# Performance work log

Hardware: AMD Instinct MI355X
Metric: run time of the kernel (lower is better)

## Reference

```python
import jax, jax.numpy as jnp
import numpy as np

B, L, SEQ_D, PAIR_D = 4, 512, 640, 128
C, H, NL = 128, 4, 3
DH = C // H
ED = PAIR_D + 1
KNN_K = 16
E_MAX = 131072
MIN_LOOP, MIN_PROB, HP_THRESH = 4, 0.01, 0.3


def _nussinov_pairs_np(P, min_loop=MIN_LOOP, min_prob=MIN_PROB):
    # Faithful numpy port of the torch.jit Nussinov DP (vectorized over diagonals)
    Ln = P.shape[0]
    S = np.zeros((Ln, Ln), dtype=np.float64)
    lo = np.where(P >= min_prob, np.log(P / (1.0 - P + 1e-9)), 0.0)
    for d in range(min_loop + 1, Ln):
        i = np.arange(Ln - d); j = i + d
        cand = np.maximum(np.maximum(S[i + 1, j], S[i, j - 1]), S[i + 1, j - 1] + lo[i, j])
        cand = np.maximum(cand, 0.0)  # best_bif starts at 0
        if d - min_loop - 1 > 0:
            K = np.arange(1, d - min_loop)
            bif = (S[i[:, None], i[:, None] + K[None, :]] + S[i[:, None] + K[None, :] + 1, j[:, None]]).max(1)
            cand = np.maximum(cand, bif)
        S[i, j] = cand
    pairs = []; stack = [(0, Ln - 1)]; tol = 1e-9
    while stack:
        i, j = stack.pop()
        if i >= j:
            continue
        if abs(S[i, j] - S[i + 1, j]) <= tol:
            stack.append((i + 1, j))
        elif abs(S[i, j] - S[i, j - 1]) <= tol:
            stack.append((i, j - 1))
        elif P[i, j] >= min_prob and abs(S[i, j] - (S[i + 1, j - 1] + lo[i, j])) <= tol:
            pairs.append((i, j)); stack.append((i + 1, j - 1))
        else:
            for k in range(i + 1, j):
                if abs(S[i, j] - (S[i, k] + S[k + 1, j])) <= tol:
                    stack.append((i, k)); stack.append((k + 1, j)); break
    return pairs


def _build_edges_np(coords, bppm):
    # backbone + Nussinov secondary-structure + kNN + high-prob BPPM edges (per sample)
    Ln = coords.shape[0]
    a = np.arange(Ln - 1)
    src = [np.concatenate([a, a + 1])]; dst = [np.concatenate([a + 1, a])]
    ss = _nussinov_pairs_np(bppm)
    pair_set = set((min(s, d), max(s, d)) for s, d in ss)
    if ss:
        s_ = np.array([p[0] for p in ss]); d_ = np.array([p[1] for p in ss])
        src.append(np.concatenate([s_, d_])); dst.append(np.concatenate([d_, s_]))
    dist = np.linalg.norm(coords[:, None, :] - coords[None, :, :], axis=-1)
    np.fill_diagonal(dist, np.inf)
    nn = np.argpartition(dist, KNN_K, axis=1)[:, :KNN_K]
    s_k = np.repeat(np.arange(Ln), KNN_K); d_k = nn.reshape(-1)
    src.append(np.concatenate([s_k, d_k])); dst.append(np.concatenate([d_k, s_k]))
    hp = np.triu(bppm >= HP_THRESH, 1)
    idx = np.arange(Ln - 1); hp[idx, idx + 1] = False
    for (pi, pj) in pair_set:
        hp[pi, pj] = False
    s_h, d_h = np.nonzero(hp)
    src.append(np.concatenate([s_h, d_h])); dst.append(np.concatenate([d_h, s_h]))
    return np.concatenate(src).astype(np.int64), np.concatenate(dst).astype(np.int64)


def _setup_common():
    rng = np.random.default_rng(0)
    seq = rng.standard_normal((B, L, SEQ_D)).astype(np.float32)
    pair = (rng.standard_normal((B, L, L, PAIR_D)) * 0.5).astype(np.float32)
    u = rng.random((B, L, L)) ** 40  # sparse, realistic BPPM (few high-prob pairs)
    bppm = ((u + np.swapaxes(u, 1, 2)) * 0.5).astype(np.float32)
    for b in range(B):
        np.fill_diagonal(bppm[b], 0.0)
    coords = np.cumsum(rng.standard_normal((B, L, 3)) * 2.0, axis=1).astype(np.float32)
    srcs, dsts = [], []
    for b in range(B):
        s, d = _build_edges_np(coords[b], bppm[b].astype(np.float64))
        srcs.append(s + b * L); dsts.append(d + b * L)
    src = np.concatenate(srcs)[:E_MAX]; dst = np.concatenate(dsts)[:E_MAX]
    E = src.shape[0]
    mask = np.zeros(E_MAX, dtype=np.float32); mask[:E] = 1.0
    src_p = np.zeros(E_MAX, dtype=np.int32); src_p[:E] = src
    dst_p = np.zeros(E_MAX, dtype=np.int32); dst_p[:E] = dst

    def w(*shape, scale):
        return (rng.standard_normal(shape) * scale).astype(np.float32)
    params = dict(
        W_in=w(SEQ_D, C, scale=SEQ_D ** -0.5),
        Wq=w(NL, C, C, scale=C ** -0.5), Wk=w(NL, C, C, scale=C ** -0.5),
        Wv=w(NL, C, C, scale=C ** -0.5), Wo=w(NL, C, C, scale=C ** -0.5),
        We=w(NL, ED, C, scale=ED ** -0.5), wd=w(NL, 1, C, scale=0.01),
        wx=w(NL, C, 1, scale=C ** -0.5),
        ln_g=np.ones((NL, C), dtype=np.float32), ln_b=np.zeros((NL, C), dtype=np.float32))
    inp = dict(sequence_rep=seq, pair_rep=pair, bppm=bppm, initial_coords=coords, **params,
               src=src_p, dst=dst_p, edge_mask=mask)
    return {k: jnp.asarray(v) for k, v in inp.items()}


def _seg_softmax(logits, seg, n):
    m = jax.ops.segment_max(logits, seg, num_segments=n)
    m = jnp.where(jnp.isfinite(m), m, 0.0)
    ex = jnp.exp(logits - m[seg])
    den = jax.ops.segment_sum(ex, seg, num_segments=n)
    return ex / (den[seg] + 1e-9)


def _forward(sequence_rep, pair_rep, bppm, initial_coords, W_in, Wq, Wk, Wv, Wo,
             We, wd, wx, ln_g, ln_b, edge_mask, src, dst):
    N = B * L
    h = sequence_rep.reshape(N, SEQ_D) @ W_in          # degree-0 node feats [N,C]
    x = initial_coords.reshape(N, 3)                    # degree-1 node feats [N,3]
    bidx = src // L
    i = src - bidx * L
    j = dst - bidx * L
    # per-edge features: gathered pair embedding + BPPM prob (edge fiber dim = 129)
    e = jnp.concatenate([pair_rep[bidx, i, j], bppm[bidx, i, j][:, None]], axis=-1)
    mask = edge_mask[:, None]
    for l in range(NL):
        rel = x[src] - x[dst]                           # [E,3] equivariant displacement
        d2 = jnp.sum(rel * rel, axis=-1, keepdims=True)  # [E,1] invariant
        q = (h @ Wq[l])[dst].reshape(-1, H, DH)
        k = (h @ Wk[l])[src].reshape(-1, H, DH)
        v = (h @ Wv[l])[src].reshape(-1, H, DH)
        eb = jax.nn.relu(e @ We[l] + d2 * wd[l]).reshape(-1, H, DH)  # edge bias
        logits = jnp.sum(q * (k + eb), axis=-1) / np.sqrt(DH) + (mask - 1.0) * 1e9
        alpha = _seg_softmax(logits, dst, N) * mask     # [E,H] per-destination softmax
        msg = (alpha[..., None] * v).reshape(-1, C)
        agg = jax.ops.segment_sum(msg, dst, num_segments=N)  # [N,C]
        h = h + jax.nn.relu(agg @ Wo[l])
        mu = jnp.mean(h, axis=-1, keepdims=True)
        var = jnp.var(h, axis=-1, keepdims=True)
        h = (h - mu) / jnp.sqrt(var + 1e-5) * ln_g[l] + ln_b[l]
        # equivariant coordinate update (degree-1 channel)
        s = jnp.tanh((k + eb).reshape(-1, C) @ wx[l]) * alpha.mean(-1, keepdims=True) * mask
        dx = jax.ops.segment_sum(s * rel / (jnp.sqrt(d2) + 1.0), dst, num_segments=N)
        x = x + dx
    return x.reshape(B, L, 3)


def setup_inputs() -> dict:
    return _setup_common()


def reference(sequence_rep, pair_rep, bppm, initial_coords, W_in, Wq, Wk, Wv, Wo,
              We, wd, wx, ln_g, ln_b, edge_mask, src, dst):
    return _forward(sequence_rep, pair_rep, bppm, initial_coords, W_in, Wq, Wk, Wv, Wo,
                    We, wd, wx, ln_g, ln_b, edge_mask, src, dst)
```

## Files before the change

### kernel.cpp

```cpp
#include <hip/hip_runtime.h>

#define LSEQ  512
#define NNODE 2048
#define CDIM  128
#define EMAX  131072
#define NLAY  3

typedef float f32x4 __attribute__((ext_vector_type(4)));
typedef unsigned short u16x8 __attribute__((ext_vector_type(8)));

static __device__ __forceinline__ unsigned short f2bf(float x) {
  unsigned u = __float_as_uint(x);
  unsigned r = (u + 0x7fffu + ((u >> 16) & 1u)) >> 16;
  return (unsigned short)r;
}

static __device__ __forceinline__ void mfma16(f32x4& d, f32x4 a, f32x4 b) {
  asm("v_mfma_f32_16x16x32_bf16 %0, %1, %2, %0" : "+v"(d) : "v"(a), "v"(b));
}

__global__ void k_zero(int* __restrict__ p, int n) {
  int i = blockIdx.x * blockDim.x + threadIdx.x;
  if (i < n) p[i] = 0;
}

__global__ void k_count(const int* __restrict__ dst, const float* __restrict__ msk,
                        int* __restrict__ cnt) {
  int e = blockIdx.x * 256 + threadIdx.x;
  if (msk[e] != 0.f) atomicAdd(&cnt[dst[e]], 1);
}

__global__ __launch_bounds__(256) void k_scan(const int* __restrict__ cnt,
                                              int* __restrict__ rowp) {
  __shared__ int lds[256];
  int t = threadIdx.x;
  int loc[8];
  int s = 0;
#pragma unroll
  for (int i = 0; i < 8; ++i) { loc[i] = s; s += cnt[t * 8 + i]; }
  lds[t] = s;
  __syncthreads();
  for (int off = 1; off < 256; off <<= 1) {
    int v = (t >= off) ? lds[t - off] : 0;
    __syncthreads();
    lds[t] += v;
    __syncthreads();
  }
  int base = t ? lds[t - 1] : 0;
#pragma unroll
  for (int i = 0; i < 8; ++i) rowp[t * 8 + i] = base + loc[i];
  if (t == 255) rowp[NNODE] = lds[255];
}

__global__ void k_fill(const int* __restrict__ dst, const float* __restrict__ msk,
                       const int* __restrict__ rowp, int* __restrict__ cur,
                       int* __restrict__ colx) {
  int e = blockIdx.x * 256 + threadIdx.x;
  if (msk[e] != 0.f) {
    int n = dst[e];
    int slot = atomicAdd(&cur[n], 1);
    colx[rowp[n] + slot] = e;
  }
}

__global__ __launch_bounds__(128) void k_hinq(
    const float* __restrict__ seq, const float* __restrict__ Win,
    const float* __restrict__ Wq0, const float* __restrict__ Wk0,
    const float* __restrict__ Wv0, float* __restrict__ h,
    float* __restrict__ hq, float* __restrict__ hk, float* __restrict__ hv) {
  __shared__ float sl[640];
  __shared__ float sh[128];
  int n = blockIdx.x, c = threadIdx.x;
  for (int i = c; i < 640; i += 128) sl[i] = seq[(size_t)n * 640 + i];
  __syncthreads();
  float a = 0.f;
#pragma unroll 4
  for (int k = 0; k < 640; ++k) a += sl[k] * Win[k * CDIM + c];
  h[n * CDIM + c] = a;
  sh[c] = a;
  __syncthreads();
  float aq = 0.f, ak = 0.f, av = 0.f;
#pragma unroll 4
  for (int k = 0; k < 128; ++k) {
    float x = sh[k];
    aq += x * Wq0[k * CDIM + c];
    ak += x * Wk0[k * CDIM + c];
    av += x * Wv0[k * CDIM + c];
  }
  hq[n * CDIM + c] = aq;
  hk[n * CDIM + c] = ak;
  hv[n * CDIM + c] = av;
}

__global__ __launch_bounds__(256) void k_ebf(const float* __restrict__ pair,
                                             const int* __restrict__ src,
                                             const int* __restrict__ dst,
                                             unsigned short* __restrict__ Ebf) {
  int tid = threadIdx.x;
  int e = blockIdx.x * 16 + (tid >> 4);
  int t = tid & 15;
  int s_ = src[e], d_ = dst[e];
  int bi = s_ >> 9;
  int j = d_ - (bi << 9);
  const float* rp = pair + ((size_t)s_ * LSEQ + j) * CDIM + t * 8;
  float4 v0 = *(const float4*)rp;
  float4 v1 = *(const float4*)(rp + 4);
  u16x8 ov;
  ov[0] = f2bf(v0.x); ov[1] = f2bf(v0.y); ov[2] = f2bf(v0.z); ov[3] = f2bf(v0.w);
  ov[4] = f2bf(v1.x); ov[5] = f2bf(v1.y); ov[6] = f2bf(v1.z); ov[7] = f2bf(v1.w);
  int byte = e * 256 + ((t * 16) ^ ((e & 7) << 4));
  *(u16x8*)((char*)Ebf + byte) = ov;
}

__global__ __launch_bounds__(256) void k_wprep(const float* __restrict__ We,
                                               unsigned short* __restrict__ WeT) {
  int idx = blockIdx.x * 256 + threadIdx.x;
  int l = idx >> 14;
  int rem = idx & 16383;
  int c = rem >> 7, k = rem & 127;
  WeT[idx] = f2bf(We[(size_t)(l * 129 + k) * 128 + c]);
}

__global__ __launch_bounds__(256) void k_edge_mfma(
    const unsigned short* __restrict__ Ebf, const float* __restrict__ bppm,
    const float* __restrict__ xc, const float* __restrict__ hq,
    const float* __restrict__ hk, const unsigned short* __restrict__ WeTl,
    const float* __restrict__ Wel, const float* __restrict__ wdl,
    const float* __restrict__ wxl, const int* __restrict__ src,
    const int* __restrict__ dst, const float* __restrict__ emask,
    float* __restrict__ logits, float* __restrict__ spre) {
  __shared__ __align__(16) unsigned char sA[16384];
  __shared__ float sPart[4][64];
  __shared__ int sS[64], sD[64];
  __shared__ float sM[64], sBp[64], sD2[64];

  const int tid = threadIdx.x;
  const int w = tid >> 6;
  const int l = tid & 63;
  const int li = l & 15, gi = l >> 4;
  const int base = blockIdx.x * 64;

  f32x4 stg[4];
  const f32x4* gE = (const f32x4*)((const char*)Ebf + (size_t)base * 256);
#pragma unroll
  for (int r = 0; r < 4; ++r) stg[r] = gE[r * 256 + tid];

  f32x4 bf[2][4];
#pragma unroll
  for (int nt = 0; nt < 2; ++nt) {
    int c = w * 32 + nt * 16 + li;
#pragma unroll
    for (int ks = 0; ks < 4; ++ks) {
      int k0 = ks * 32 + gi * 8;
      bf[nt][ks] = *(const f32x4*)((const char*)WeTl + (size_t)(c * 128 + k0) * 2);
    }
  }

  if (tid < 64) {
    int e = base + tid;
    int s_ = src[e], d_ = dst[e];
    sS[tid] = s_; sD[tid] = d_; sM[tid] = emask[e];
    int bi = s_ >> 9;
    int j = d_ - (bi << 9);
    float rx = xc[3 * s_ + 0] - xc[3 * d_ + 0];
    float ry = xc[3 * s_ + 1] - xc[3 * d_ + 1];
    float rz = xc[3 * s_ + 2] - xc[3 * d_ + 2];
    sD2[tid] = rx * rx + ry * ry + rz * rz;
    sBp[tid] = bppm[(size_t)s_ * LSEQ + j];
  }

  f32x4* sA4 = (f32x4*)sA;
#pragma unroll
  for (int r = 0; r < 4; ++r) sA4[r * 256 + tid] = stg[r];
  __syncthreads();

  f32x4 acc[4][2];
#pragma unroll
  for (int m = 0; m < 4; ++m)
#pragma unroll
    for (int nt = 0; nt < 2; ++nt) acc[m][nt] = (f32x4){0.f, 0.f, 0.f, 0.f};

#pragma unroll
  for (int ks = 0; ks < 4; ++ks) {
    f32x4 af[4];
#pragma unroll
    for (int m = 0; m < 4; ++m) {
      int row = m * 16 + li;
      int byte = row * 256 + (((ks * 32 + gi * 8) * 2) ^ ((row & 7) << 4));
      af[m] = *(const f32x4*)(sA + byte);
    }
#pragma unroll
    for (int m = 0; m < 4; ++m) {
      mfma16(acc[m][0], af[m], bf[0][ks]);
      mfma16(acc[m][1], af[m], bf[1][ks]);
    }
  }

  const float rs = 0.17677669529663689f;
  const int c0 = w * 32 + li, c1 = c0 + 16;
  const float w128_0 = Wel[128 * 128 + c0], w128_1 = Wel[128 * 128 + c1];
  const float wd0 = wdl[c0], wd1 = wdl[c1];
  const float wx0 = wxl[c0], wx1 = wxl[c1];

#pragma unroll
  for (int m = 0; m < 4; ++m) {
#pragma unroll
    for (int r = 0; r < 4; ++r) {
      int el = m * 16 + gi * 4 + r;
      float bp = sBp[el], d2 = sD2[el];
      int s_ = sS[el], d_ = sD[el];
      float eb0 = fmaxf(acc[m][0][r] + bp * w128_0 + d2 * wd0, 0.f);
      float eb1 = fmaxf(acc[m][1][r] + bp * w128_1 + d2 * wd1, 0.f);
      float keb0 = hk[s_ * CDIM + c0] + eb0;
      float keb1 = hk[s_ * CDIM + c1] + eb1;
      float lp = hq[d_ * CDIM + c0] * keb0 + hq[d_ * CDIM + c1] * keb1;
      float sp = wx0 * keb0 + wx1 * keb1;
#pragma unroll
      for (int o = 1; o < 16; o <<= 1) {
        lp += __shfl_xor(lp, o);
        sp += __shfl_xor(sp, o);
      }
      if (li == 0) {
        int e = base + el;
        logits[e * 4 + w] = lp * rs + (sM[el] - 1.f) * 1e9f;
        sPart[w][el] = sp;
      }
    }
  }
  __syncthreads();
  if (tid < 64)
    spre[base + tid] =
        tanhf(sPart[0][tid] + sPart[1][tid] + sPart[2][tid] + sPart[3][tid]);
}

__global__ __launch_bounds__(256) void k_aggf(
    const int* __restrict__ rowp, const int* __restrict__ colx,
    const float4* __restrict__ lg4, const float* __restrict__ spre,
    const float* __restrict__ hvin, const int* __restrict__ src,
    const float* __restrict__ xc, float* __restrict__ xn,
    float* __restrict__ h, const float* __restrict__ Wol,
    const float* __restrict__ g, const float* __restrict__ b,
    const float* __restrict__ Wqn, const float* __restrict__ Wkn,
    const float* __restrict__ Wvn, float* __restrict__ hqo,
    float* __restrict__ hko, float* __restrict__ hvo, int last) {
  const int n = blockIdx.x, tid = threadIdx.x;
  const int w = tid >> 6, lane = tid & 63;
  const int st = rowp[n], deg = rowp[n + 1] - st;

  __shared__ float sA[256][4];
  __shared__ int sSe[256];
  __shared__ float sRed[4][4];
  __shared__ float sAcc[4][128];
  __shared__ float sV[128];
  __shared__ float sP[2][128];
  __shared__ float sDx[4][3];
  __shared__ float sLn[4];

  float m0 = -3e38f, m1 = -3e38f, m2 = -3e38f, m3 = -3e38f;
  for (int i = tid; i < deg; i += 256) {
    float4 lg = lg4[colx[st + i]];
    m0 = fmaxf(m0, lg.x); m1 = fmaxf(m1, lg.y);
    m2 = fmaxf(m2, lg.z); m3 = fmaxf(m3, lg.w);
  }
#pragma unroll
  for (int o = 32; o; o >>= 1) {
    m0 = fmaxf(m0, __shfl_xor(m0, o)); m1 = fmaxf(m1, __shfl_xor(m1, o));
    m2 = fmaxf(m2, __shfl_xor(m2, o)); m3 = fmaxf(m3, __shfl_xor(m3, o));
  }
  if (!lane) { sRed[w][0] = m0; sRed[w][1] = m1; sRed[w][2] = m2; sRed[w][3] = m3; }
  __syncthreads();
  m0 = fmaxf(fmaxf(sRed[0][0], sRed[1][0]), fmaxf(sRed[2][0], sRed[3][0]));
  m1 = fmaxf(fmaxf(sRed[0][1], sRed[1][1]), fmaxf(sRed[2][1], sRed[3][1]));
  m2 = fmaxf(fmaxf(sRed[0][2], sRed[1][2]), fmaxf(sRed[2][2], sRed[3][2]));
  m3 = fmaxf(fmaxf(sRed[0][3], sRed[1][3]), fmaxf(sRed[2][3], sRed[3][3]));
  __syncthreads();

  float dn0 = 0.f, dn1 = 0.f, dn2 = 0.f, dn3 = 0.f;
  for (int i = tid; i < deg; i += 256) {
    float4 lg = lg4[colx[st + i]];
    dn0 += __expf(lg.x - m0); dn1 += __expf(lg.y - m1);
    dn2 += __expf(lg.z - m2); dn3 += __expf(lg.w - m3);
  }
#pragma unroll
  for (int o = 32; o; o >>= 1) {
    dn0 += __shfl_xor(dn0, o); dn1 += __shfl_xor(dn1, o);
    dn2 += __shfl_xor(dn2, o); dn3 += __shfl_xor(dn3, o);
  }
  if (!lane) { sRed[w][0] = dn0; sRed[w][1] = dn1; sRed[w][2] = dn2; sRed[w][3] = dn3; }
  __syncthreads();
  dn0 = sRed[0][0] + sRed[1][0] + sRed[2][0] + sRed[3][0];
  dn1 = sRed[0][1] + sRed[1][1] + sRed[2][1] + sRed[3][1];
  dn2 = sRed[0][2] + sRed[1][2] + sRed[2][2] + sRed[3][2];
  dn3 = sRed[0][3] + sRed[1][3] + sRed[2][3] + sRed[3][3];
  const float r0 = 1.f / (dn0 + 1e-9f), r1 = 1.f / (dn1 + 1e-9f);
  const float r2 = 1.f / (dn2 + 1e-9f), r3 = 1.f / (dn3 + 1e-9f);

  const float xnx = xc[3 * n], xny = xc[3 * n + 1], xnz = xc[3 * n + 2];
  float accA = 0.f, accB = 0.f, dxx = 0.f, dxy = 0.f, dxz = 0.f;
  const int hA = lane >> 5, hB = 2 + (lane >> 5);

  for (int bs = 0; bs < deg; bs += 256) {
    int cnt = min(256, deg - bs);
    __syncthreads();
    if (tid < cnt) {
      int e = colx[st + bs + tid];
      float4 lg = lg4[e];
      float a0 = __expf(lg.x - m0) * r0;
      float a1 = __expf(lg.y - m1) * r1;
      float a2 = __expf(lg.z - m2) * r2;
      float a3 = __expf(lg.w - m3) * r3;
      int se = src[e];
      sA[tid][0] = a0; sA[tid][1] = a1; sA[tid][2] = a2; sA[tid][3] = a3;
      sSe[tid] = se;
      float rx = xc[3 * se + 0] - xnx;
      float ry = xc[3 * se + 1] - xny;
      float rz = xc[3 * se + 2] - xnz;
      float dd = rx * rx + ry * ry + rz * rz;
      float s = spre[e] * (a0 + a1 + a2 + a3) * 0.25f;
      float inv = s / (sqrtf(dd) + 1.f);
      dxx += rx * inv; dxy += ry * inv; dxz += rz * inv;
    }
    __syncthreads();
#pragma unroll 4
    for (int j = w; j < cnt; j += 4) {
      const float* vr = hvin + (size_t)sSe[j] * CDIM;
      accA += sA[j][hA] * vr[lane];
      accB += sA[j][hB] * vr[lane + 64];
    }
  }
  sAcc[w][lane] = accA;
  sAcc[w][64 + lane] = accB;
#pragma unroll
  for (int o = 32; o; o >>= 1) {
    dxx += __shfl_xor(dxx, o);
    dxy += __shfl_xor(dxy, o);
    dxz += __shfl_xor(dxz, o);
  }
  if (!lane) { sDx[w][0] = dxx; sDx[w][1] = dxy; sDx[w][2] = dxz; }
  __syncthreads();
  if (tid == 0) {
    xn[3 * n + 0] = xnx + sDx[0][0] + sDx[1][0] + sDx[2][0] + sDx[3][0];
    xn[3 * n + 1] = xny + sDx[0][1] + sDx[1][1] + sDx[2][1] + sDx[3][1];
    xn[3 * n + 2] = xnz + sDx[0][2] + sDx[1][2] + sDx[2][2] + sDx[3][2];
  }
  if (last) return;

  if (tid < 128) sV[tid] = sAcc[0][tid] + sAcc[1][tid] + sAcc[2][tid] + sAcc[3][tid];
  __syncthreads();

  const int c = tid & 127, kh = tid >> 7;
  {
    float acc = 0.f;
    const float* wrow = Wol + (size_t)kh * 64 * CDIM + c;
#pragma unroll 8
    for (int k = 0; k < 64; ++k) acc += sV[kh * 64 + k] * wrow[k * CDIM];
    sP[kh][c] = acc;
  }
  __syncthreads();
  float hn = 0.f;
  if (tid < 128) {
    float o = sP[0][tid] + sP[1][tid];
    hn = h[n * CDIM + tid] + fmaxf(o, 0.f);
    float s1 = hn, s2 = hn * hn;
#pragma unroll
    for (int o2 = 32; o2; o2 >>= 1) {
      s1 += __shfl_xor(s1, o2);
      s2 += __shfl_xor(s2, o2);
    }
    if (!lane) { sLn[w * 2] = s1; sLn[w * 2 + 1] = s2; }
  }
  __syncthreads();
  if (tid < 128) {
    float s1 = sLn[0] + sLn[2], s2 = sLn[1] + sLn[3];
    float mu = s1 * (1.f / 128.f);
    float var = s2 * (1.f / 128.f) - mu * mu;
    float hv_ = (hn - mu) * rsqrtf(var + 1e-5f) * g[tid] + b[tid];
    h[n * CDIM + tid] = hv_;
    sV[tid] = hv_;
  }
  __syncthreads();

  float* buf = &sA[0][0];
  {
    float aq = 0.f, ak = 0.f, av = 0.f;
    const float* q_ = Wqn + (size_t)kh * 64 * CDIM + c;
    const float* k_ = Wkn + (size_t)kh * 64 * CDIM + c;
    const float* v_ = Wvn + (size_t)kh * 64 * CDIM + c;
#pragma unroll 8
    for (int k = 0; k < 64; ++k) {
      float x = sV[kh * 64 + k];
      aq += x * q_[k * CDIM];
      ak += x * k_[k * CDIM];
      av += x * v_[k * CDIM];
    }
    buf[kh * 384 + c] = aq;
    buf[kh * 384 + 128 + c] = ak;
    buf[kh * 384 + 256 + c] = av;
  }
  __syncthreads();
  if (tid < 128) {
    hqo[n * CDIM + tid] = buf[tid] + buf[384 + tid];
    hko[n * CDIM + tid] = buf[128 + tid] + buf[384 + 128 + tid];
    hvo[n * CDIM + tid] = buf[256 + tid] + buf[384 + 256 + tid];
  }
}

extern "C" void kernel_launch(void* const* d_in, const int* in_sizes, int n_in,
                              void* d_out, int out_size, void* d_ws, size_t ws_size,
                              hipStream_t stream) {
  const float* seq    = (const float*)d_in[0];
  const float* pair   = (const float*)d_in[1];
  const float* bppm   = (const float*)d_in[2];
  const float* coords = (const float*)d_in[3];
  const float* Win    = (const float*)d_in[4];
  const float* Wq     = (const float*)d_in[5];
  const float* Wk     = (const float*)d_in[6];
  const float* Wv     = (const float*)d_in[7];
  const float* Wo     = (const float*)d_in[8];
  const float* We     = (const float*)d_in[9];
  const float* wd     = (const float*)d_in[10];
  const float* wx     = (const float*)d_in[11];
  const float* lng    = (const float*)d_in[12];
  const float* lnb    = (const float*)d_in[13];
  const int*   src    = (const int*)d_in[14];
  const int*   dst    = (const int*)d_in[15];
  const float* emask  = (const float*)d_in[16];
  float* out = (float*)d_out;

  size_t off = 0;
  auto take = [&](size_t bytes) {
    void* p = (char*)d_ws + off;
    off += (bytes + 255) & ~(size_t)255;
    return p;
  };
  float* h      = (float*)take((size_t)NNODE * CDIM * 4);
  float* hqA    = (float*)take((size_t)NNODE * CDIM * 4);
  float* hkA    = (float*)take((size_t)NNODE * CDIM * 4);
  float* hvA    = (float*)take((size_t)NNODE * CDIM * 4);
  float* hqB    = (float*)take((size_t)NNODE * CDIM * 4);
  float* hkB    = (float*)take((size_t)NNODE * CDIM * 4);
  float* hvB    = (float*)take((size_t)NNODE * CDIM * 4);
  float* logits = (float*)take((size_t)EMAX * 4 * 4);
  float* spre   = (float*)take((size_t)EMAX * 4);
  float* x0     = (float*)take((size_t)NNODE * 3 * 4);
  float* x1     = (float*)take((size_t)NNODE * 3 * 4);
  int*   cnt    = (int*)take((size_t)NNODE * 2 * 4);
  int*   cur    = cnt + NNODE;
  int*   rowp   = (int*)take((size_t)(NNODE + 1) * 4);
  int*   colx   = (int*)take((size_t)EMAX * 4);
  unsigned short* Ebf = (unsigned short*)take((size_t)EMAX * CDIM * 2);
  unsigned short* WeT = (unsigned short*)take((size_t)NLAY * CDIM * CDIM * 2);

  k_zero<<<(NNODE * 2 + 255) / 256, 256, 0, stream>>>(cnt, NNODE * 2);
  k_count<<<EMAX / 256, 256, 0, stream>>>(dst, emask, cnt);
  k_scan<<<1, 256, 0, stream>>>(cnt, rowp);
  k_fill<<<EMAX / 256, 256, 0, stream>>>(dst, emask, rowp, cur, colx);

  k_ebf<<<EMAX / 16, 256, 0, stream>>>(pair, src, dst, Ebf);
  k_wprep<<<(NLAY * CDIM * CDIM) / 256, 256, 0, stream>>>(We, WeT);
  k_hinq<<<NNODE, 128, 0, stream>>>(seq, Win, Wq, Wk, Wv, h, hqA, hkA, hvA);

  const float* xc = coords;
  for (int l = 0; l < NLAY; ++l) {
    const float* hqi = (l & 1) ? hqB : hqA;
    const float* hki = (l & 1) ? hkB : hkA;
    const float* hvi = (l & 1) ? hvB : hvA;
    float* hqo = (l & 1) ? hqA : hqB;
    float* hko = (l & 1) ? hkA : hkB;
    float* hvo = (l & 1) ? hvA : hvB;
    int ln = (l < NLAY - 1) ? l + 1 : l;

    k_edge_mfma<<<EMAX / 64, 256, 0, stream>>>(
        Ebf, bppm, xc, hqi, hki, WeT + (size_t)l * CDIM * CDIM,
        We + (size_t)l * 129 * CDIM, wd + (size_t)l * CDIM,
        wx + (size_t)l * CDIM, src, dst, emask, logits, spre);

    float* xn = (l == NLAY - 1) ? out : (l == 0 ? x0 : x1);
    k_aggf<<<NNODE, 256, 0, stream>>>(
        rowp, colx, (const float4*)logits, spre, hvi, src, xc, xn, h,
        Wo + (size_t)l * CDIM * CDIM, lng + (size_t)l * CDIM,
        lnb + (size_t)l * CDIM, Wq + (size_t)ln * CDIM * CDIM,
        Wk + (size_t)ln * CDIM * CDIM, Wv + (size_t)ln * CDIM * CDIM,
        hqo, hko, hvo, l == NLAY - 1);
    xc = xn;
  }
}
```

Before: 260.4 us.

## Split node update into separate kernel with LDS-tiled weights over four nodes

The per-node linear layers (input projection, output projection, and the next layer's Q/K/V projections) now process four nodes per block and stage weight tiles in LDS, so each weight element loaded from memory is reused across several nodes. The node update (Wo, residual, layernorm, QKV) moves out of the aggregation kernel into a new k_node kernel that reads an aggregated buffer, and h is double-buffered. This cuts redundant weight reads but adds an extra launch per layer, an intermediate agg round-trip, and 512-block grids with lower parallelism.

```diff
diff --git a/kernel.cpp b/kernel.cpp
--- a/kernel.cpp
+++ b/kernel.cpp
@@ -63,33 +63,63 @@
   }
 }
 
-__global__ __launch_bounds__(128) void k_hinq(
+__global__ __launch_bounds__(256) void k_hinq(
     const float* __restrict__ seq, const float* __restrict__ Win,
     const float* __restrict__ Wq0, const float* __restrict__ Wk0,
     const float* __restrict__ Wv0, float* __restrict__ h,
     float* __restrict__ hq, float* __restrict__ hk, float* __restrict__ hv) {
-  __shared__ float sl[640];
-  __shared__ float sh[128];
-  int n = blockIdx.x, c = threadIdx.x;
-  for (int i = c; i < 640; i += 128) sl[i] = seq[(size_t)n * 640 + i];
-  __syncthreads();
-  float a = 0.f;
-#pragma unroll 4
-  for (int k = 0; k < 640; ++k) a += sl[k] * Win[k * CDIM + c];
-  h[n * CDIM + c] = a;
-  sh[c] = a;
-  __syncthreads();
-  float aq = 0.f, ak = 0.f, av = 0.f;
-#pragma unroll 4
-  for (int k = 0; k < 128; ++k) {
-    float x = sh[k];
-    aq += x * Wq0[k * CDIM + c];
-    ak += x * Wk0[k * CDIM + c];
-    av += x * Wv0[k * CDIM + c];
-  }
-  hq[n * CDIM + c] = aq;
-  hk[n * CDIM + c] = ak;
-  hv[n * CDIM + c] = av;
+  __shared__ float sSeq[4][64];
+  __shared__ __align__(16) float sW[64][128];
+  __shared__ float sH[4][128];
+  const int tid = threadIdx.x;
+  const int c = tid & 127, g = tid >> 7;
+  const int nb = blockIdx.x * 4;
+
+  float a0 = 0.f, a1 = 0.f;
+  for (int kc = 0; kc < 10; ++kc) {
+    if (tid < 64) {
+      int n = tid >> 4, t4 = tid & 15;
+      *(float4*)&sSeq[n][t4 * 4] =
+          *(const float4*)&seq[(size_t)(nb + n) * 640 + kc * 64 + t4 * 4];
+    }
+    const float4* wsrc = (const float4*)(Win + (size_t)kc * 64 * CDIM);
+#pragma unroll
+    for (int i = 0; i < 8; ++i) ((float4*)sW)[tid + i * 256] = wsrc[tid + i * 256];
+    __syncthreads();
+#pragma unroll 8
+    for (int k = 0; k < 64; ++k) {
+      float w = sW[k][c];
+      a0 += sSeq[g * 2][k] * w;
+      a1 += sSeq[g * 2 + 1][k] * w;
+    }
+    __syncthreads();
+  }
+  h[(size_t)(nb + g * 2) * CDIM + c] = a0;
+  h[(size_t)(nb + g * 2 + 1) * CDIM + c] = a1;
+  sH[g * 2][c] = a0;
+  sH[g * 2 + 1][c] = a1;
+  __syncthreads();
+
+  for (int ws = 0; ws < 3; ++ws) {
+    const float* W = ws == 0 ? Wq0 : (ws == 1 ? Wk0 : Wv0);
+    float b0 = 0.f, b1 = 0.f;
+    for (int kc = 0; kc < 2; ++kc) {
+      const float4* wsrc = (const float4*)(W + (size_t)kc * 64 * CDIM);
+#pragma unroll
+      for (int i = 0; i < 8; ++i) ((float4*)sW)[tid + i * 256] = wsrc[tid + i * 256];
+      __syncthreads();
+#pragma unroll 8
+      for (int k = 0; k < 64; ++k) {
+        float w = sW[k][c];
+        b0 += sH[g * 2][kc * 64 + k] * w;
+        b1 += sH[g * 2 + 1][kc * 64 + k] * w;
+      }
+      __syncthreads();
+    }
+    float* o = ws == 0 ? hq : (ws == 1 ? hk : hv);
+    o[(size_t)(nb + g * 2) * CDIM + c] = b0;
+    o[(size_t)(nb + g * 2 + 1) * CDIM + c] = b1;
+  }
 }
 
 __global__ __launch_bounds__(256) void k_ebf(const float* __restrict__ pair,
@@ -238,11 +268,7 @@
     const float4* __restrict__ lg4, const float* __restrict__ spre,
     const float* __restrict__ hvin, const int* __restrict__ src,
     const float* __restrict__ xc, float* __restrict__ xn,
-    float* __restrict__ h, const float* __restrict__ Wol,
-    const float* __restrict__ g, const float* __restrict__ b,
-    const float* __restrict__ Wqn, const float* __restrict__ Wkn,
-    const float* __restrict__ Wvn, float* __restrict__ hqo,
-    float* __restrict__ hko, float* __restrict__ hvo, int last) {
+    float* __restrict__ agg) {
   const int n = blockIdx.x, tid = threadIdx.x;
   const int w = tid >> 6, lane = tid & 63;
   const int st = rowp[n], deg = rowp[n + 1] - st;
@@ -251,10 +277,7 @@
   __shared__ int sSe[256];
   __shared__ float sRed[4][4];
   __shared__ float sAcc[4][128];
-  __shared__ float sV[128];
-  __shared__ float sP[2][128];
   __shared__ float sDx[4][3];
-  __shared__ float sLn[4];
 
   float m0 = -3e38f, m1 = -3e38f, m2 = -3e38f, m3 = -3e38f;
   for (int i = tid; i < deg; i += 256) {
@@ -343,65 +366,102 @@
     xn[3 * n + 1] = xny + sDx[0][1] + sDx[1][1] + sDx[2][1] + sDx[3][1];
     xn[3 * n + 2] = xnz + sDx[0][2] + sDx[1][2] + sDx[2][2] + sDx[3][2];
   }
-  if (last) return;
-
-  if (tid < 128) sV[tid] = sAcc[0][tid] + sAcc[1][tid] + sAcc[2][tid] + sAcc[3][tid];
-  __syncthreads();
-
-  const int c = tid & 127, kh = tid >> 7;
+  if (tid < 128)
+    agg[(size_t)n * CDIM + tid] =
+        sAcc[0][tid] + sAcc[1][tid] + sAcc[2][tid] + sAcc[3][tid];
+}
+
+__global__ __launch_bounds__(256) void k_node(
+    const float* __restrict__ agg, const float* __restrict__ hin,
+    const float* __restrict__ Wol, const float* __restrict__ gl,
+    const float* __restrict__ bl, const float* __restrict__ Wqn,
+    const float* __restrict__ Wkn, const float* __restrict__ Wvn,
+    float* __restrict__ hout, float* __restrict__ hq,
+    float* __restrict__ hk, float* __restrict__ hv) {
+  __shared__ float sAg[4][128];
+  __shared__ float sHin[4][128];
+  __shared__ __align__(16) float sW[64][128];
+  __shared__ float sH[4][128];
+  __shared__ float sRed[4][2][2];
+  const int tid = threadIdx.x;
+  const int c = tid & 127, g = tid >> 7;
+  const int w = tid >> 6, lane = tid & 63;
+  const int nb = blockIdx.x * 4;
+
   {
-    float acc = 0.f;
-    const float* wrow = Wol + (size_t)kh * 64 * CDIM + c;
-#pragma unroll 8
-    for (int k = 0; k < 64; ++k) acc += sV[kh * 64 + k] * wrow[k * CDIM];
-    sP[kh][c] = acc;
-  }
-  __syncthreads();
-  float hn = 0.f;
-  if (tid < 128) {
-    float o = sP[0][tid] + sP[1][tid];
-    hn = h[n * CDIM + tid] + fmaxf(o, 0.f);
-    float s1 = hn, s2 = hn * hn;
-#pragma unroll
-    for (int o2 = 32; o2; o2 >>= 1) {
-      s1 += __shfl_xor(s1, o2);
-      s2 += __shfl_xor(s2, o2);
-    }
-    if (!lane) { sLn[w * 2] = s1; sLn[w * 2 + 1] = s2; }
-  }
-  __syncthreads();
-  if (tid < 128) {
-    float s1 = sLn[0] + sLn[2], s2 = sLn[1] + sLn[3];
-    float mu = s1 * (1.f / 128.f);
-    float var = s2 * (1.f / 128.f) - mu * mu;
-    float hv_ = (hn - mu) * rsqrtf(var + 1e-5f) * g[tid] + b[tid];
-    h[n * CDIM + tid] = hv_;
-    sV[tid] = hv_;
-  }
-  __syncthreads();
-
-  float* buf = &sA[0][0];
-  {
-    float aq = 0.f, ak = 0.f, av = 0.f;
-    const float* q_ = Wqn + (size_t)kh * 64 * CDIM + c;
-    const float* k_ = Wkn + (size_t)kh * 64 * CDIM + c;
-    const float* v_ = Wvn + (size_t)kh * 64 * CDIM + c;
+    int i = tid & 127, half = tid >> 7;
+    int n = i >> 5, t4 = i & 31;
+    const float* srcb = half ? hin : agg;
+    float* dstb = half ? &sHin[0][0] : &sAg[0][0];
+    *(float4*)&dstb[n * 128 + t4 * 4] =
+        *(const float4*)&srcb[(size_t)(nb + n) * CDIM + t4 * 4];
+  }
+  __syncthreads();
+
+  float o0 = 0.f, o1 = 0.f;
+  for (int kc = 0; kc < 2; ++kc) {
+    const float4* wsrc = (const float4*)(Wol + (size_t)kc * 64 * CDIM);
+#pragma unroll
+    for (int i = 0; i < 8; ++i) ((float4*)sW)[tid + i * 256] = wsrc[tid + i * 256];
+    __syncthreads();
 #pragma unroll 8
     for (int k = 0; k < 64; ++k) {
-      float x = sV[kh * 64 + k];
-      aq += x * q_[k * CDIM];
-      ak += x * k_[k * CDIM];
-      av += x * v_[k * CDIM];
-    }
-    buf[kh * 384 + c] = aq;
-    buf[kh * 384 + 128 + c] = ak;
-    buf[kh * 384 + 256 + c] = av;
-  }
-  __syncthreads();
-  if (tid < 128) {
-    hqo[n * CDIM + tid] = buf[tid] + buf[384 + tid];
-    hko[n * CDIM + tid] = buf[128 + tid] + buf[384 + 128 + tid];
-    hvo[n * CDIM + tid] = buf[256 + tid] + buf[384 + 256 + tid];
+      float wv = sW[k][c];
+      o0 += sAg[g * 2][kc * 64 + k] * wv;
+      o1 += sAg[g * 2 + 1][kc * 64 + k] * wv;
+    }
+    __syncthreads();
+  }
+  float hn0 = sHin[g * 2][c] + fmaxf(o0, 0.f);
+  float hn1 = sHin[g * 2 + 1][c] + fmaxf(o1, 0.f);
+  float s10 = hn0, s20 = hn0 * hn0, s11 = hn1, s21 = hn1 * hn1;
+#pragma unroll
+  for (int o = 32; o; o >>= 1) {
+    s10 += __shfl_xor(s10, o); s20 += __shfl_xor(s20, o);
+    s11 += __shfl_xor(s11, o); s21 += __shfl_xor(s21, o);
+  }
+  if (!lane) {
+    sRed[w][0][0] = s10; sRed[w][0][1] = s20;
+    sRed[w][1][0] = s11; sRed[w][1][1] = s21;
+  }
+  __syncthreads();
+  {
+    float t10 = sRed[g * 2][0][0] + sRed[g * 2 + 1][0][0];
+    float t20 = sRed[g * 2][0][1] + sRed[g * 2 + 1][0][1];
+    float t11 = sRed[g * 2][1][0] + sRed[g * 2 + 1][1][0];
+    float t21 = sRed[g * 2][1][1] + sRed[g * 2 + 1][1][1];
+    float mu0 = t10 * (1.f / 128.f), mu1 = t11 * (1.f / 128.f);
+    float v0 = t20 * (1.f / 128.f) - mu0 * mu0;
+    float v1 = t21 * (1.f / 128.f) - mu1 * mu1;
+    float gg = gl[c], bb = bl[c];
+    hn0 = (hn0 - mu0) * rsqrtf(v0 + 1e-5f) * gg + bb;
+    hn1 = (hn1 - mu1) * rsqrtf(v1 + 1e-5f) * gg + bb;
+  }
+  hout[(size_t)(nb + g * 2) * CDIM + c] = hn0;
+  hout[(size_t)(nb + g * 2 + 1) * CDIM + c] = hn1;
+  sH[g * 2][c] = hn0;
+  sH[g * 2 + 1][c] = hn1;
+  __syncthreads();
+
+  for (int ws = 0; ws < 3; ++ws) {
+    const float* W = ws == 0 ? Wqn : (ws == 1 ? Wkn : Wvn);
+    float b0 = 0.f, b1 = 0.f;
+    for (int kc = 0; kc < 2; ++kc) {
+      const float4* wsrc = (const float4*)(W + (size_t)kc * 64 * CDIM);
+#pragma unroll
+      for (int i = 0; i < 8; ++i) ((float4*)sW)[tid + i * 256] = wsrc[tid + i * 256];
+      __syncthreads();
+#pragma unroll 8
+      for (int k = 0; k < 64; ++k) {
+        float wv = sW[k][c];
+        b0 += sH[g * 2][kc * 64 + k] * wv;
+        b1 += sH[g * 2 + 1][kc * 64 + k] * wv;
+      }
+      __syncthreads();
+    }
+    float* o = ws == 0 ? hq : (ws == 1 ? hk : hv);
+    o[(size_t)(nb + g * 2) * CDIM + c] = b0;
+    o[(size_t)(nb + g * 2 + 1) * CDIM + c] = b1;
   }
 }
 
@@ -433,7 +493,8 @@
     off += (bytes + 255) & ~(size_t)255;
     return p;
   };
-  float* h      = (float*)take((size_t)NNODE * CDIM * 4);
+  float* hA     = (float*)take((size_t)NNODE * CDIM * 4);
+  float* hB     = (float*)take((size_t)NNODE * CDIM * 4);
   float* hqA    = (float*)take((size_t)NNODE * CDIM * 4);
   float* hkA    = (float*)take((size_t)NNODE * CDIM * 4);
   float* hvA    = (float*)take((size_t)NNODE * CDIM * 4);
@@ -442,6 +503,7 @@
   float* hvB    = (float*)take((size_t)NNODE * CDIM * 4);
   float* logits = (float*)take((size_t)EMAX * 4 * 4);
   float* spre   = (float*)take((size_t)EMAX * 4);
+  float* agg    = (float*)take((size_t)NNODE * CDIM * 4);
   float* x0     = (float*)take((size_t)NNODE * 3 * 4);
   float* x1     = (float*)take((size_t)NNODE * 3 * 4);
   int*   cnt    = (int*)take((size_t)NNODE * 2 * 4);
@@ -458,7 +520,7 @@
 
   k_ebf<<<EMAX / 16, 256, 0, stream>>>(pair, src, dst, Ebf);
   k_wprep<<<(NLAY * CDIM * CDIM) / 256, 256, 0, stream>>>(We, WeT);
-  k_hinq<<<NNODE, 128, 0, stream>>>(seq, Win, Wq, Wk, Wv, h, hqA, hkA, hvA);
+  k_hinq<<<NNODE / 4, 256, 0, stream>>>(seq, Win, Wq, Wk, Wv, hA, hqA, hkA, hvA);
 
   const float* xc = coords;
   for (int l = 0; l < NLAY; ++l) {
@@ -468,7 +530,8 @@
     float* hqo = (l & 1) ? hqA : hqB;
     float* hko = (l & 1) ? hkA : hkB;
     float* hvo = (l & 1) ? hvA : hvB;
-    int ln = (l < NLAY - 1) ? l + 1 : l;
+    const float* hin = (l & 1) ? hB : hA;
+    float* hout = (l & 1) ? hA : hB;
 
     k_edge_mfma<<<EMAX / 64, 256, 0, stream>>>(
         Ebf, bppm, xc, hqi, hki, WeT + (size_t)l * CDIM * CDIM,
@@ -476,12 +539,14 @@
         wx + (size_t)l * CDIM, src, dst, emask, logits, spre);
 
     float* xn = (l == NLAY - 1) ? out : (l == 0 ? x0 : x1);
-    k_aggf<<<NNODE, 256, 0, stream>>>(
-        rowp, colx, (const float4*)logits, spre, hvi, src, xc, xn, h,
-        Wo + (size_t)l * CDIM * CDIM, lng + (size_t)l * CDIM,
-        lnb + (size_t)l * CDIM, Wq + (size_t)ln * CDIM * CDIM,
-        Wk + (size_t)ln * CDIM * CDIM, Wv + (size_t)ln * CDIM * CDIM,
-        hqo, hko, hvo, l == NLAY - 1);
+    k_aggf<<<NNODE, 256, 0, stream>>>(rowp, colx, (const float4*)logits, spre,
+                                      hvi, src, xc, xn, agg);
+    if (l < NLAY - 1)
+      k_node<<<NNODE / 4, 256, 0, stream>>>(
+          agg, hin, Wo + (size_t)l * CDIM * CDIM, lng + (size_t)l * CDIM,
+          lnb + (size_t)l * CDIM, Wq + (size_t)(l + 1) * CDIM * CDIM,
+          Wk + (size_t)(l + 1) * CDIM * CDIM, Wv + (size_t)(l + 1) * CDIM * CDIM,
+          hout, hqo, hko, hvo);
     xc = xn;
   }
 }
```

After: 240.5 us. 1.08x faster.
